# Kernel tuning notes

Measured on AMD Instinct MI355X. Metric: run time of the kernel, lower is better.

## Reference

```python
import jax, jax.numpy as jnp
import numpy as np

NUM_HEADS = 16
HEAD_DIM = 64
Q_DIM = K_DIM = V_DIM = 1024
LQ = LK = 4096
TAU = HEAD_DIM ** (-0.5)


def setup_inputs() -> dict:
    key = jax.random.key(0)
    ks = jax.random.split(key, 11)
    inner = NUM_HEADS * HEAD_DIM
    s = 0.02
    return {
        "q": jax.random.normal(ks[0], (LQ, Q_DIM), dtype=jnp.float32),
        "k": jax.random.normal(ks[1], (LK, K_DIM), dtype=jnp.float32),
        "v": jax.random.normal(ks[2], (LK, V_DIM), dtype=jnp.float32),
        "Wq": jax.random.normal(ks[3], (Q_DIM, inner), dtype=jnp.float32) * s,
        "bq": jax.random.normal(ks[4], (inner,), dtype=jnp.float32) * s,
        "Wk": jax.random.normal(ks[5], (K_DIM, inner), dtype=jnp.float32) * s,
        "bk": jax.random.normal(ks[6], (inner,), dtype=jnp.float32) * s,
        "Wv": jax.random.normal(ks[7], (V_DIM, inner), dtype=jnp.float32) * s,
        "bv": jax.random.normal(ks[8], (inner,), dtype=jnp.float32) * s,
        "Wo": jax.random.normal(ks[9], (inner, Q_DIM), dtype=jnp.float32) * s,
        "bo": jax.random.normal(ks[10], (Q_DIM,), dtype=jnp.float32) * s,
    }


def reference(q, k, v, Wq, bq, Wk, bk, Wv, bv, Wo, bo):
    h, x = NUM_HEADS, HEAD_DIM
    # projections: [L, h*x] -> per-head layout
    qh = (q @ Wq + bq).reshape(-1, h, x)  # [Lq, h, x]
    kh = (k @ Wk + bk).reshape(-1, h, x)  # [Lk, h, x]
    vh = (v @ Wv + bv).reshape(-1, h, x)  # [Lk, h, x]
    # scores: [h, Lq, Lk]
    att = jnp.einsum('qhx,khx->hqk', qh, kh) * TAU
    att = jax.nn.softmax(att, axis=-1)  # dropout=0.0 -> identity
    ctx = jnp.einsum('hqk,khx->qhx', att, vh).reshape(-1, h * x)  # [Lq, h*x]
    out = ctx @ Wo + bo  # [Lq, Q_DIM]
    return out, att
```

## Files before the change

kernel.cpp:

```cpp
#include <hip/hip_runtime.h>
#include <hip/hip_bf16.h>

typedef unsigned short ushort_t;
typedef __attribute__((ext_vector_type(8))) short short8;
typedef __attribute__((ext_vector_type(8))) __bf16 bf16x8;
typedef __attribute__((ext_vector_type(4))) float f32x4;

#define LQS 4096
#define LKS 4096
#define NH 16
#define HD 64
#define DIN 1024
#define KVB 64
static constexpr float TAU_S = 0.125f;
static constexpr float LOG2E = 1.4426950408889634f;

__device__ __forceinline__ float exp2_fast(float x) { return __builtin_amdgcn_exp2f(x); }
__device__ __forceinline__ float log2_fast(float x) { return __builtin_amdgcn_logf(x); }

__device__ __forceinline__ ushort_t f32_to_bf16(float x) {
  union { float f; unsigned u; } v; v.f = x;
  unsigned r = v.u + 0x7FFF + ((v.u >> 16) & 1);
  return (ushort_t)(r >> 16);
}

__device__ __forceinline__ unsigned cvt_pk_bf16(float a, float b) {
  unsigned r;
  asm volatile("v_cvt_pk_bf16_f32 %0, %1, %2" : "=v"(r) : "v"(a), "v"(b));
  return r;
}

__device__ __forceinline__ void gld_lds16(const void* g, void* l) {
  __builtin_amdgcn_global_load_lds((const __attribute__((address_space(1))) void*)g,
                                   (__attribute__((address_space(3))) void*)l, 16, 0, 0);
}

__device__ __forceinline__ f32x4 mfma16(bf16x8 a, bf16x8 b, f32x4 c) {
  return __builtin_amdgcn_mfma_f32_16x16x32_bf16(a, b, c, 0, 0, 0);
}

struct Cvt3 { const float* src[3]; ushort_t* dst[3]; };
__global__ void cvt_kernel(Cvt3 c) {
  const float* __restrict__ src = c.src[blockIdx.y];
  ushort_t* __restrict__ dst = c.dst[blockIdx.y];
  int i = (blockIdx.x * 256 + threadIdx.x) * 8;
  float4 a = *(const float4*)(src + i);
  float4 b = *(const float4*)(src + i + 4);
  union { unsigned w[4]; short8 s; } o;
  o.w[0] = cvt_pk_bf16(a.x, a.y);
  o.w[1] = cvt_pk_bf16(a.z, a.w);
  o.w[2] = cvt_pk_bf16(b.x, b.y);
  o.w[3] = cvt_pk_bf16(b.z, b.w);
  *(short8*)(dst + i) = o.s;
}

struct TW4 { const float* W[4]; ushort_t* Wt[4]; };
__global__ void transpose_w(TW4 w) {
  const float* __restrict__ W = w.W[blockIdx.z];
  ushort_t* __restrict__ Wt = w.Wt[blockIdx.z];
  __shared__ float tile[64][65];
  const int t = threadIdx.x;
  const int k0 = blockIdx.y * 64, n0 = blockIdx.x * 64;
#pragma unroll
  for (int i = 0; i < 16; ++i) {
    int idx = i * 256 + t;
    int r = idx >> 6, c = idx & 63;
    tile[r][c] = W[(size_t)(k0 + r) * DIN + n0 + c];
  }
  __syncthreads();
#pragma unroll
  for (int i = 0; i < 16; ++i) {
    int idx = i * 256 + t;
    int r = idx >> 6, c = idx & 63;
    Wt[(size_t)(n0 + r) * DIN + k0 + c] = f32_to_bf16(tile[c][r]);
  }
}

__global__ void transpose_v(const ushort_t* __restrict__ vh, ushort_t* __restrict__ vt) {
  __shared__ ushort_t tile[64][65];
  const int t = threadIdx.x;
  const int k0 = blockIdx.x * 64, h = blockIdx.y;
#pragma unroll
  for (int i = 0; i < 16; ++i) {
    int idx = i * 256 + t;
    int r = idx >> 6, c = idx & 63;
    tile[r][c] = vh[(size_t)(k0 + r) * DIN + h * HD + c];
  }
  __syncthreads();
#pragma unroll
  for (int i = 0; i < 16; ++i) {
    int idx = i * 256 + t;
    int r = idx >> 6, c = idx & 63;
    vt[((size_t)h * HD + r) * (size_t)LKS + k0 + c] = tile[c][r];
  }
}

struct Batch3 {
  const ushort_t* A[3];
  const ushort_t* Bt[3];
  const float* bias[3];
  void* C[3];
  float scale[3];
};
template <bool OUT_F32>
__launch_bounds__(256, 2)
__global__ void gemm_nt(Batch3 bt3) {
  const int bid = blockIdx.x;
  const int xcd = bid & 7, idx = bid >> 3;
  const int z = idx >> 5, rem = idx & 31;
  const int by = xcd * 4 + (rem >> 3), bx = rem & 7;
  const ushort_t* __restrict__ A = bt3.A[z];
  const ushort_t* __restrict__ Bt = bt3.Bt[z];
  const float* __restrict__ bias = bt3.bias[z];
  void* __restrict__ Cout = bt3.C[z];
  const float scale = bt3.scale[z];
  const int K = DIN, N = DIN;

  __shared__ __align__(16) ushort_t Alds[128 * 64];
  __shared__ __align__(16) ushort_t Blds[128 * 64];
  const int t = threadIdx.x, wave = t >> 6, lane = t & 63;
  const int l15 = lane & 15, lg = lane >> 4;
  const int m0 = by * 128, n0 = bx * 128;
  const int wr = wave >> 1, wc = wave & 1;
  f32x4 acc[4][4];
#pragma unroll
  for (int i = 0; i < 4; ++i)
#pragma unroll
    for (int j = 0; j < 4; ++j) acc[i][j] = (f32x4){0.f, 0.f, 0.f, 0.f};

  for (int tk = 0; tk < K / 64; ++tk) {
#pragma unroll
    for (int c = 0; c < 4; ++c) {
      int chunk = wave * 4 + c;
      int row = chunk * 8 + (lane >> 3);
      int ss = (lane & 7) ^ (row & 7);
      gld_lds16(A + (size_t)(m0 + row) * K + tk * 64 + ss * 8, (char*)Alds + chunk * 1024);
      gld_lds16(Bt + (size_t)(n0 + row) * K + tk * 64 + ss * 8, (char*)Blds + chunk * 1024);
    }
    __syncthreads();
#pragma unroll
    for (int kk = 0; kk < 2; ++kk) {
      bf16x8 a[4], b[4];
#pragma unroll
      for (int i = 0; i < 4; ++i) {
        int ra = wr * 64 + i * 16 + l15;
        a[i] = *(const bf16x8*)((const char*)Alds + ra * 128 + ((((kk * 4 + lg) << 4)) ^ ((ra & 7) << 4)));
        int rb = wc * 64 + i * 16 + l15;
        b[i] = *(const bf16x8*)((const char*)Blds + rb * 128 + ((((kk * 4 + lg) << 4)) ^ ((rb & 7) << 4)));
      }
#pragma unroll
      for (int mi = 0; mi < 4; ++mi)
#pragma unroll
        for (int ni = 0; ni < 4; ++ni)
          acc[mi][ni] = mfma16(a[mi], b[ni], acc[mi][ni]);
    }
    __syncthreads();
  }
#pragma unroll
  for (int ni = 0; ni < 4; ++ni) {
    int coln = n0 + wc * 64 + ni * 16 + l15;
    float bv = bias[coln];
#pragma unroll
    for (int mi = 0; mi < 4; ++mi) {
#pragma unroll
      for (int r = 0; r < 4; ++r) {
        int rowm = m0 + wr * 64 + mi * 16 + lg * 4 + r;
        float v = (acc[mi][ni][r] + bv) * scale;
        if (OUT_F32)
          ((float*)Cout)[(size_t)rowm * N + coln] = v;
        else
          ((ushort_t*)Cout)[(size_t)rowm * N + coln] = f32_to_bf16(v);
      }
    }
  }
}

__launch_bounds__(256, 2)
__global__ void attn_kernel(const ushort_t* __restrict__ qh, const ushort_t* __restrict__ kh,
                            const ushort_t* __restrict__ vt, float* __restrict__ att,
                            ushort_t* __restrict__ ctx) {
  __shared__ __align__(16) ushort_t Klds[2][KVB * 64];
  __shared__ __align__(16) ushort_t Vlds[2][KVB * 64];
  const int t = threadIdx.x, wave = t >> 6, lane = t & 63;
  const int l15 = lane & 15, lg = lane >> 4;
  const int bid = blockIdx.x;
  const int xcd = bid & 7, idx = bid >> 3;
  const int h = xcd * 2 + (idx >> 5);
  const int q0 = (idx & 31) * 128;
  const int w0 = q0 + wave * 32;

  bf16x8 qa[2][2];
#pragma unroll
  for (int g = 0; g < 2; ++g) {
    const ushort_t* qp = qh + (size_t)(w0 + g * 16 + l15) * DIN + h * HD + lg * 8;
    qa[g][0] = *(const bf16x8*)(qp);
    qa[g][1] = *(const bf16x8*)(qp + 32);
  }

  const int srow8 = lane >> 3;
  const int sslot = (lane & 7);

  float rs[2] = {0.f, 0.f};
  for (int tk = 0; tk < LKS / (2 * KVB); ++tk) {
#pragma unroll
    for (int sub = 0; sub < 2; ++sub) {
#pragma unroll
      for (int c = 0; c < 2; ++c) {
        int chunk = wave * 2 + c;
        int row = chunk * 8 + srow8;
        int ss = sslot ^ (row & 7);
        gld_lds16(kh + (size_t)((tk * 2 + sub) * KVB + row) * DIN + h * HD + ss * 8,
                  (char*)Klds[sub] + chunk * 1024);
      }
    }
    __syncthreads();
#pragma unroll
    for (int sub = 0; sub < 2; ++sub) {
#pragma unroll
      for (int ct = 0; ct < 4; ++ct) {
        f32x4 a0 = (f32x4){0.f, 0.f, 0.f, 0.f};
        f32x4 a1 = (f32x4){0.f, 0.f, 0.f, 0.f};
#pragma unroll
        for (int kk = 0; kk < 2; ++kk) {
          int row = ct * 16 + l15;
          bf16x8 kb = *(const bf16x8*)((const char*)Klds[sub] + row * 128 + ((((kk * 4 + lg) << 4)) ^ ((row & 7) << 4)));
          a0 = mfma16(kb, qa[0][kk], a0);
          a1 = mfma16(kb, qa[1][kk], a1);
        }
#pragma unroll
        for (int r = 0; r < 4; ++r) {
          rs[0] += exp2_fast(a0[r]);
          rs[1] += exp2_fast(a1[r]);
        }
      }
    }
    __syncthreads();
  }
  float lrs[2];
#pragma unroll
  for (int g = 0; g < 2; ++g) {
    rs[g] += __shfl_xor(rs[g], 16, 64);
    rs[g] += __shfl_xor(rs[g], 32, 64);
    lrs[g] = log2_fast(rs[g]);
  }

  f32x4 cacc[2][4];
#pragma unroll
  for (int g = 0; g < 2; ++g)
#pragma unroll
    for (int x = 0; x < 4; ++x) cacc[g][x] = (f32x4){0.f, 0.f, 0.f, 0.f};
  float* atth = att + ((size_t)h << 24);

  for (int tk = 0; tk < LKS / (2 * KVB); ++tk) {
#pragma unroll
    for (int sub = 0; sub < 2; ++sub) {
#pragma unroll
      for (int c = 0; c < 2; ++c) {
        int chunk = wave * 2 + c;
        int row = chunk * 8 + srow8;
        int ss = sslot ^ (row & 7);
        gld_lds16(kh + (size_t)((tk * 2 + sub) * KVB + row) * DIN + h * HD + ss * 8,
                  (char*)Klds[sub] + chunk * 1024);
        gld_lds16(vt + ((size_t)h * HD + row) * (size_t)LKS + (tk * 2 + sub) * KVB + ss * 8,
                  (char*)Vlds[sub] + chunk * 1024);
      }
    }
    __syncthreads();
#pragma unroll
    for (int sub = 0; sub < 2; ++sub) {
      float p[2][4][4];
#pragma unroll
      for (int ct = 0; ct < 4; ++ct) {
        f32x4 a0 = (f32x4){0.f, 0.f, 0.f, 0.f};
        f32x4 a1 = (f32x4){0.f, 0.f, 0.f, 0.f};
#pragma unroll
        for (int kk = 0; kk < 2; ++kk) {
          int row = ct * 16 + l15;
          bf16x8 kb = *(const bf16x8*)((const char*)Klds[sub] + row * 128 + ((((kk * 4 + lg) << 4)) ^ ((row & 7) << 4)));
          a0 = mfma16(kb, qa[0][kk], a0);
          a1 = mfma16(kb, qa[1][kk], a1);
        }
#pragma unroll
        for (int r = 0; r < 4; ++r) {
          p[0][ct][r] = exp2_fast(a0[r] - lrs[0]);
          p[1][ct][r] = exp2_fast(a1[r] - lrs[1]);
        }
      }
#pragma unroll
      for (int g = 0; g < 2; ++g) {
#pragma unroll
        for (int ct = 0; ct < 4; ++ct) {
          f32x4 v = (f32x4){p[g][ct][0], p[g][ct][1], p[g][ct][2], p[g][ct][3]};
          *(f32x4*)(atth + (((size_t)(w0 + g * 16 + l15)) << 12) + (tk * 2 + sub) * KVB + ct * 16 + lg * 4) = v;
        }
      }
      bf16x8 pa[2][2];
#pragma unroll
      for (int g = 0; g < 2; ++g)
#pragma unroll
        for (int kk = 0; kk < 2; ++kk) {
          union { unsigned w[4]; bf16x8 v; } P;
          P.w[0] = cvt_pk_bf16(p[g][2 * kk][0], p[g][2 * kk][1]);
          P.w[1] = cvt_pk_bf16(p[g][2 * kk][2], p[g][2 * kk][3]);
          P.w[2] = cvt_pk_bf16(p[g][2 * kk + 1][0], p[g][2 * kk + 1][1]);
          P.w[3] = cvt_pk_bf16(p[g][2 * kk + 1][2], p[g][2 * kk + 1][3]);
          pa[g][kk] = P.v;
        }
#pragma unroll
      for (int x = 0; x < 4; ++x) {
        int row = x * 16 + l15;
        const char* vrow = (const char*)Vlds[sub] + row * 128;
        int par = row & 7;
        int sb = (lg & 1) << 3;
#pragma unroll
        for (int kk = 0; kk < 2; ++kk) {
          int sA = (4 * kk + (lg >> 1)) ^ par;
          int sB = (4 * kk + 2 + (lg >> 1)) ^ par;
          union { unsigned long long q[2]; bf16x8 v; } U;
          U.q[0] = *(const unsigned long long*)(vrow + (sA << 4) + sb);
          U.q[1] = *(const unsigned long long*)(vrow + (sB << 4) + sb);
          cacc[0][x] = mfma16(pa[0][kk], U.v, cacc[0][x]);
          cacc[1][x] = mfma16(pa[1][kk], U.v, cacc[1][x]);
        }
      }
    }
    __syncthreads();
  }
#pragma unroll
  for (int g = 0; g < 2; ++g)
#pragma unroll
    for (int x = 0; x < 4; ++x) {
#pragma unroll
      for (int r = 0; r < 4; ++r) {
        int rowq = w0 + g * 16 + lg * 4 + r;
        int col = h * HD + x * 16 + l15;
        ctx[(size_t)rowq * DIN + col] = f32_to_bf16(cacc[g][x][r]);
      }
    }
}

extern "C" void kernel_launch(void* const* d_in, const int* in_sizes, int n_in,
                              void* d_out, int out_size, void* d_ws, size_t ws_size,
                              hipStream_t stream) {
  const float* q = (const float*)d_in[0];
  const float* k = (const float*)d_in[1];
  const float* v = (const float*)d_in[2];
  const float* Wq = (const float*)d_in[3];
  const float* bq = (const float*)d_in[4];
  const float* Wk = (const float*)d_in[5];
  const float* bk = (const float*)d_in[6];
  const float* Wv = (const float*)d_in[7];
  const float* bv = (const float*)d_in[8];
  const float* Wo = (const float*)d_in[9];
  const float* bo = (const float*)d_in[10];

  float* out = (float*)d_out;
  float* att = out + (size_t)LQS * DIN;

  char* ws = (char*)d_ws;
  ushort_t* qhb = (ushort_t*)(ws + (size_t)0);
  ushort_t* khb = (ushort_t*)(ws + ((size_t)8 << 20));
  ushort_t* vhb = (ushort_t*)(ws + ((size_t)16 << 20));
  ushort_t* vtb = (ushort_t*)(ws + ((size_t)24 << 20));
  ushort_t* ctx = (ushort_t*)(ws + ((size_t)32 << 20));
  ushort_t* qb = (ushort_t*)(ws + ((size_t)40 << 20));
  ushort_t* kb = (ushort_t*)(ws + ((size_t)48 << 20));
  ushort_t* vb = (ushort_t*)(ws + ((size_t)56 << 20));
  ushort_t* Wqt = (ushort_t*)(ws + ((size_t)64 << 20));
  ushort_t* Wkt = (ushort_t*)(ws + ((size_t)66 << 20));
  ushort_t* Wvt = (ushort_t*)(ws + ((size_t)68 << 20));
  ushort_t* Wot = (ushort_t*)(ws + ((size_t)70 << 20));

  Cvt3 c3;
  c3.src[0] = q; c3.src[1] = k; c3.src[2] = v;
  c3.dst[0] = qb; c3.dst[1] = kb; c3.dst[2] = vb;
  cvt_kernel<<<dim3(LQS * DIN / 8 / 256, 3), 256, 0, stream>>>(c3);

  TW4 w4;
  w4.W[0] = Wq; w4.W[1] = Wk; w4.W[2] = Wv; w4.W[3] = Wo;
  w4.Wt[0] = Wqt; w4.Wt[1] = Wkt; w4.Wt[2] = Wvt; w4.Wt[3] = Wot;
  transpose_w<<<dim3(16, 16, 4), 256, 0, stream>>>(w4);

  Batch3 pb;
  pb.A[0] = qb; pb.A[1] = kb; pb.A[2] = vb;
  pb.Bt[0] = Wqt; pb.Bt[1] = Wkt; pb.Bt[2] = Wvt;
  pb.bias[0] = bq; pb.bias[1] = bk; pb.bias[2] = bv;
  pb.C[0] = qhb; pb.C[1] = khb; pb.C[2] = vhb;
  pb.scale[0] = TAU_S * LOG2E; pb.scale[1] = 1.0f; pb.scale[2] = 1.0f;
  gemm_nt<false><<<768, 256, 0, stream>>>(pb);

  transpose_v<<<dim3(64, 16), 256, 0, stream>>>(vhb, vtb);

  attn_kernel<<<512, 256, 0, stream>>>(qhb, khb, vtb, att, ctx);

  Batch3 ob;
  ob.A[0] = ctx; ob.A[1] = ctx; ob.A[2] = ctx;
  ob.Bt[0] = Wot; ob.Bt[1] = Wot; ob.Bt[2] = Wot;
  ob.bias[0] = bo; ob.bias[1] = bo; ob.bias[2] = bo;
  ob.C[0] = out; ob.C[1] = out; ob.C[2] = out;
  ob.scale[0] = 1.0f; ob.scale[1] = 1.0f; ob.scale[2] = 1.0f;
  gemm_nt<true><<<256, 256, 0, stream>>>(ob);
}
```

Before: 391.6 us.

## Double-buffer K/V tiles and give each wave 64 query rows in attention

The attention kernel now stages the next K (and V) tile into the alternate LDS buffer while computing on the current one, replacing the previous load-then-sync pattern. Each wave handles 64 query rows instead of 32, so each K/V tile loaded into LDS is reused across twice as many rows, and the grid shrinks from 512 to 256 blocks. Launch bounds drop to one block per CU to allow the extra registers. This reduces K/V reloads and exposes less memory latency, at the cost of lower occupancy and a grid of only 256 blocks, which may leave some CUs idle on a large GPU.

```diff
diff --git a/kernel.cpp b/kernel.cpp
--- a/kernel.cpp
+++ b/kernel.cpp
@@ -175,7 +175,7 @@
   }
 }
 
-__launch_bounds__(256, 2)
+__launch_bounds__(256, 1)
 __global__ void attn_kernel(const ushort_t* __restrict__ qh, const ushort_t* __restrict__ kh,
                             const ushort_t* __restrict__ vt, float* __restrict__ att,
                             ushort_t* __restrict__ ctx) {
@@ -185,13 +185,13 @@
   const int l15 = lane & 15, lg = lane >> 4;
   const int bid = blockIdx.x;
   const int xcd = bid & 7, idx = bid >> 3;
-  const int h = xcd * 2 + (idx >> 5);
-  const int q0 = (idx & 31) * 128;
-  const int w0 = q0 + wave * 32;
-
-  bf16x8 qa[2][2];
-#pragma unroll
-  for (int g = 0; g < 2; ++g) {
+  const int h = xcd * 2 + (idx >> 4);
+  const int q0 = (idx & 15) * 256;
+  const int w0 = q0 + wave * 64;
+
+  bf16x8 qa[4][2];
+#pragma unroll
+  for (int g = 0; g < 4; ++g) {
     const ushort_t* qp = qh + (size_t)(w0 + g * 16 + l15) * DIN + h * HD + lg * 8;
     qa[g][0] = *(const bf16x8*)(qp);
     qa[g][1] = *(const bf16x8*)(qp + 32);
@@ -199,135 +199,142 @@
 
   const int srow8 = lane >> 3;
   const int sslot = (lane & 7);
-
-  float rs[2] = {0.f, 0.f};
-  for (int tk = 0; tk < LKS / (2 * KVB); ++tk) {
-#pragma unroll
-    for (int sub = 0; sub < 2; ++sub) {
-#pragma unroll
-      for (int c = 0; c < 2; ++c) {
-        int chunk = wave * 2 + c;
-        int row = chunk * 8 + srow8;
-        int ss = sslot ^ (row & 7);
-        gld_lds16(kh + (size_t)((tk * 2 + sub) * KVB + row) * DIN + h * HD + ss * 8,
-                  (char*)Klds[sub] + chunk * 1024);
-      }
+  const int NT = LKS / KVB;
+
+#define STAGE_K(tile, buf)                                                          \
+  {                                                                                 \
+    _Pragma("unroll") for (int c = 0; c < 2; ++c) {                                 \
+      int chunk = wave * 2 + c;                                                     \
+      int row = chunk * 8 + srow8;                                                  \
+      int ss = sslot ^ (row & 7);                                                   \
+      gld_lds16(kh + (size_t)((tile) * KVB + row) * DIN + h * HD + ss * 8,          \
+                (char*)Klds[buf] + chunk * 1024);                                   \
+    }                                                                               \
+  }
+#define STAGE_V(tile, buf)                                                          \
+  {                                                                                 \
+    _Pragma("unroll") for (int c = 0; c < 2; ++c) {                                 \
+      int chunk = wave * 2 + c;                                                     \
+      int row = chunk * 8 + srow8;                                                  \
+      int ss = sslot ^ (row & 7);                                                   \
+      gld_lds16(vt + ((size_t)h * HD + row) * (size_t)LKS + (tile) * KVB + ss * 8,  \
+                (char*)Vlds[buf] + chunk * 1024);                                   \
+    }                                                                               \
+  }
+
+  float rs[4] = {0.f, 0.f, 0.f, 0.f};
+  STAGE_K(0, 0);
+  __syncthreads();
+  int cur = 0;
+  for (int tk = 0; tk < NT; ++tk) {
+    if (tk + 1 < NT) STAGE_K(tk + 1, cur ^ 1);
+#pragma unroll
+    for (int ct = 0; ct < 4; ++ct) {
+      int row = ct * 16 + l15;
+      bf16x8 kb0 = *(const bf16x8*)((const char*)Klds[cur] + row * 128 + (((lg << 4)) ^ ((row & 7) << 4)));
+      bf16x8 kb1 = *(const bf16x8*)((const char*)Klds[cur] + row * 128 + ((((4 + lg) << 4)) ^ ((row & 7) << 4)));
+      f32x4 a[4];
+#pragma unroll
+      for (int g = 0; g < 4; ++g) {
+        a[g] = mfma16(kb0, qa[g][0], (f32x4){0.f, 0.f, 0.f, 0.f});
+        a[g] = mfma16(kb1, qa[g][1], a[g]);
+      }
+#pragma unroll
+      for (int g = 0; g < 4; ++g)
+#pragma unroll
+        for (int r = 0; r < 4; ++r) rs[g] += exp2_fast(a[g][r]);
     }
     __syncthreads();
-#pragma unroll
-    for (int sub = 0; sub < 2; ++sub) {
-#pragma unroll
-      for (int ct = 0; ct < 4; ++ct) {
-        f32x4 a0 = (f32x4){0.f, 0.f, 0.f, 0.f};
-        f32x4 a1 = (f32x4){0.f, 0.f, 0.f, 0.f};
-#pragma unroll
-        for (int kk = 0; kk < 2; ++kk) {
-          int row = ct * 16 + l15;
-          bf16x8 kb = *(const bf16x8*)((const char*)Klds[sub] + row * 128 + ((((kk * 4 + lg) << 4)) ^ ((row & 7) << 4)));
-          a0 = mfma16(kb, qa[0][kk], a0);
-          a1 = mfma16(kb, qa[1][kk], a1);
-        }
-#pragma unroll
-        for (int r = 0; r < 4; ++r) {
-          rs[0] += exp2_fast(a0[r]);
-          rs[1] += exp2_fast(a1[r]);
-        }
-      }
-    }
-    __syncthreads();
-  }
-  float lrs[2];
-#pragma unroll
-  for (int g = 0; g < 2; ++g) {
+    cur ^= 1;
+  }
+  float lrs[4];
+#pragma unroll
+  for (int g = 0; g < 4; ++g) {
     rs[g] += __shfl_xor(rs[g], 16, 64);
     rs[g] += __shfl_xor(rs[g], 32, 64);
     lrs[g] = log2_fast(rs[g]);
   }
 
-  f32x4 cacc[2][4];
-#pragma unroll
-  for (int g = 0; g < 2; ++g)
+  f32x4 cacc[4][4];
+#pragma unroll
+  for (int g = 0; g < 4; ++g)
 #pragma unroll
     for (int x = 0; x < 4; ++x) cacc[g][x] = (f32x4){0.f, 0.f, 0.f, 0.f};
   float* atth = att + ((size_t)h << 24);
 
-  for (int tk = 0; tk < LKS / (2 * KVB); ++tk) {
-#pragma unroll
-    for (int sub = 0; sub < 2; ++sub) {
-#pragma unroll
-      for (int c = 0; c < 2; ++c) {
-        int chunk = wave * 2 + c;
-        int row = chunk * 8 + srow8;
-        int ss = sslot ^ (row & 7);
-        gld_lds16(kh + (size_t)((tk * 2 + sub) * KVB + row) * DIN + h * HD + ss * 8,
-                  (char*)Klds[sub] + chunk * 1024);
-        gld_lds16(vt + ((size_t)h * HD + row) * (size_t)LKS + (tk * 2 + sub) * KVB + ss * 8,
-                  (char*)Vlds[sub] + chunk * 1024);
+  STAGE_K(0, 0);
+  STAGE_V(0, 0);
+  __syncthreads();
+  cur = 0;
+  for (int tk = 0; tk < NT; ++tk) {
+    if (tk + 1 < NT) {
+      STAGE_K(tk + 1, cur ^ 1);
+      STAGE_V(tk + 1, cur ^ 1);
+    }
+    bf16x8 pa[4][2];
+    float pprev[4][4];
+#pragma unroll
+    for (int ct = 0; ct < 4; ++ct) {
+      int row = ct * 16 + l15;
+      bf16x8 kb0 = *(const bf16x8*)((const char*)Klds[cur] + row * 128 + (((lg << 4)) ^ ((row & 7) << 4)));
+      bf16x8 kb1 = *(const bf16x8*)((const char*)Klds[cur] + row * 128 + ((((4 + lg) << 4)) ^ ((row & 7) << 4)));
+      f32x4 a[4];
+#pragma unroll
+      for (int g = 0; g < 4; ++g) {
+        a[g] = mfma16(kb0, qa[g][0], (f32x4){0.f, 0.f, 0.f, 0.f});
+        a[g] = mfma16(kb1, qa[g][1], a[g]);
+      }
+      float pcur[4][4];
+#pragma unroll
+      for (int g = 0; g < 4; ++g)
+#pragma unroll
+        for (int r = 0; r < 4; ++r) pcur[g][r] = exp2_fast(a[g][r] - lrs[g]);
+#pragma unroll
+      for (int g = 0; g < 4; ++g) {
+        f32x4 v = (f32x4){pcur[g][0], pcur[g][1], pcur[g][2], pcur[g][3]};
+        *(f32x4*)(atth + (((size_t)(w0 + g * 16 + l15)) << 12) + tk * KVB + ct * 16 + lg * 4) = v;
+      }
+      if (ct & 1) {
+#pragma unroll
+        for (int g = 0; g < 4; ++g) {
+          union { unsigned w[4]; bf16x8 v; } P;
+          P.w[0] = cvt_pk_bf16(pprev[g][0], pprev[g][1]);
+          P.w[1] = cvt_pk_bf16(pprev[g][2], pprev[g][3]);
+          P.w[2] = cvt_pk_bf16(pcur[g][0], pcur[g][1]);
+          P.w[3] = cvt_pk_bf16(pcur[g][2], pcur[g][3]);
+          pa[g][ct >> 1] = P.v;
+        }
+      } else {
+#pragma unroll
+        for (int g = 0; g < 4; ++g)
+#pragma unroll
+          for (int r = 0; r < 4; ++r) pprev[g][r] = pcur[g][r];
+      }
+    }
+#pragma unroll
+    for (int x = 0; x < 4; ++x) {
+      int row = x * 16 + l15;
+      const char* vrow = (const char*)Vlds[cur] + row * 128;
+      int par = row & 7;
+      int sb = (lg & 1) << 3;
+#pragma unroll
+      for (int kk = 0; kk < 2; ++kk) {
+        int sA = (4 * kk + (lg >> 1)) ^ par;
+        int sB = (4 * kk + 2 + (lg >> 1)) ^ par;
+        union { unsigned long long q[2]; bf16x8 v; } U;
+        U.q[0] = *(const unsigned long long*)(vrow + (sA << 4) + sb);
+        U.q[1] = *(const unsigned long long*)(vrow + (sB << 4) + sb);
+#pragma unroll
+        for (int g = 0; g < 4; ++g) cacc[g][x] = mfma16(pa[g][kk], U.v, cacc[g][x]);
       }
     }
     __syncthreads();
-#pragma unroll
-    for (int sub = 0; sub < 2; ++sub) {
-      float p[2][4][4];
-#pragma unroll
-      for (int ct = 0; ct < 4; ++ct) {
-        f32x4 a0 = (f32x4){0.f, 0.f, 0.f, 0.f};
-        f32x4 a1 = (f32x4){0.f, 0.f, 0.f, 0.f};
-#pragma unroll
-        for (int kk = 0; kk < 2; ++kk) {
-          int row = ct * 16 + l15;
-          bf16x8 kb = *(const bf16x8*)((const char*)Klds[sub] + row * 128 + ((((kk * 4 + lg) << 4)) ^ ((row & 7) << 4)));
-          a0 = mfma16(kb, qa[0][kk], a0);
-          a1 = mfma16(kb, qa[1][kk], a1);
-        }
-#pragma unroll
-        for (int r = 0; r < 4; ++r) {
-          p[0][ct][r] = exp2_fast(a0[r] - lrs[0]);
-          p[1][ct][r] = exp2_fast(a1[r] - lrs[1]);
-        }
-      }
-#pragma unroll
-      for (int g = 0; g < 2; ++g) {
-#pragma unroll
-        for (int ct = 0; ct < 4; ++ct) {
-          f32x4 v = (f32x4){p[g][ct][0], p[g][ct][1], p[g][ct][2], p[g][ct][3]};
-          *(f32x4*)(atth + (((size_t)(w0 + g * 16 + l15)) << 12) + (tk * 2 + sub) * KVB + ct * 16 + lg * 4) = v;
-        }
-      }
-      bf16x8 pa[2][2];
-#pragma unroll
-      for (int g = 0; g < 2; ++g)
-#pragma unroll
-        for (int kk = 0; kk < 2; ++kk) {
-          union { unsigned w[4]; bf16x8 v; } P;
-          P.w[0] = cvt_pk_bf16(p[g][2 * kk][0], p[g][2 * kk][1]);
-          P.w[1] = cvt_pk_bf16(p[g][2 * kk][2], p[g][2 * kk][3]);
-          P.w[2] = cvt_pk_bf16(p[g][2 * kk + 1][0], p[g][2 * kk + 1][1]);
-          P.w[3] = cvt_pk_bf16(p[g][2 * kk + 1][2], p[g][2 * kk + 1][3]);
-          pa[g][kk] = P.v;
-        }
-#pragma unroll
-      for (int x = 0; x < 4; ++x) {
-        int row = x * 16 + l15;
-        const char* vrow = (const char*)Vlds[sub] + row * 128;
-        int par = row & 7;
-        int sb = (lg & 1) << 3;
-#pragma unroll
-        for (int kk = 0; kk < 2; ++kk) {
-          int sA = (4 * kk + (lg >> 1)) ^ par;
-          int sB = (4 * kk + 2 + (lg >> 1)) ^ par;
-          union { unsigned long long q[2]; bf16x8 v; } U;
-          U.q[0] = *(const unsigned long long*)(vrow + (sA << 4) + sb);
-          U.q[1] = *(const unsigned long long*)(vrow + (sB << 4) + sb);
-          cacc[0][x] = mfma16(pa[0][kk], U.v, cacc[0][x]);
-          cacc[1][x] = mfma16(pa[1][kk], U.v, cacc[1][x]);
-        }
-      }
-    }
-    __syncthreads();
-  }
-#pragma unroll
-  for (int g = 0; g < 2; ++g)
+    cur ^= 1;
+  }
+#undef STAGE_K
+#undef STAGE_V
+#pragma unroll
+  for (int g = 0; g < 4; ++g)
 #pragma unroll
     for (int x = 0; x < 4; ++x) {
 #pragma unroll
@@ -391,7 +398,7 @@
 
   transpose_v<<<dim3(64, 16), 256, 0, stream>>>(vhb, vtb);
 
-  attn_kernel<<<512, 256, 0, stream>>>(qhb, khb, vtb, att, ctx);
+  attn_kernel<<<256, 256, 0, stream>>>(qhb, khb, vtb, att, ctx);
 
   Batch3 ob;
   ob.A[0] = ctx; ob.A[1] = ctx; ob.A[2] = ctx;
```

Result: slower. 554.8 us (+41.7%).

## Split softmax row-sum pass into separate kernel with larger Q tiles and split-K

Applied to the files above, without the earlier changes.

Moves the first pass of attention, which computes softmax denominators without max subtraction, out of attn_kernel into a new rowsum_kernel. Each wave now handles 64 query rows, so every loaded K tile feeds more MFMAs. Each block covers half of the key range, with the two partial sums written to a workspace buffer. The new kernel also double-buffers K loads into shared memory so the next tile loads during compute. attn_kernel reads the two partial sums and takes their log, at the cost of one more launch and a small global buffer.

```diff
diff --git a/kernel.cpp b/kernel.cpp
--- a/kernel.cpp
+++ b/kernel.cpp
@@ -176,9 +176,84 @@
 }
 
 __launch_bounds__(256, 2)
+__global__ void rowsum_kernel(const ushort_t* __restrict__ qh, const ushort_t* __restrict__ kh,
+                              float* __restrict__ rsbuf) {
+  __shared__ __align__(16) ushort_t Klds[2][KVB * 64];
+  const int t = threadIdx.x, wave = t >> 6, lane = t & 63;
+  const int l15 = lane & 15, lg = lane >> 4;
+  const int bid = blockIdx.x;
+  const int xcd = bid & 7, idx = bid >> 3;
+  const int h = xcd * 2 + (idx >> 5);
+  const int rem = idx & 31;
+  const int q0 = (rem >> 1) * 256;
+  const int half = rem & 1;
+  const int w0 = q0 + wave * 64;
+
+  bf16x8 qa[4][2];
+#pragma unroll
+  for (int g = 0; g < 4; ++g) {
+    const ushort_t* qp = qh + (size_t)(w0 + g * 16 + l15) * DIN + h * HD + lg * 8;
+    qa[g][0] = *(const bf16x8*)(qp);
+    qa[g][1] = *(const bf16x8*)(qp + 32);
+  }
+
+  const int srow8 = lane >> 3;
+  const int sslot = (lane & 7);
+  const int tk0 = half * 32;
+
+#define STAGE_K1(tile, buf)                                                         \
+  {                                                                                 \
+    _Pragma("unroll") for (int c = 0; c < 2; ++c) {                                 \
+      int chunk = wave * 2 + c;                                                     \
+      int row = chunk * 8 + srow8;                                                  \
+      int ss = sslot ^ (row & 7);                                                   \
+      gld_lds16(kh + (size_t)((tile) * KVB + row) * DIN + h * HD + ss * 8,          \
+                (char*)Klds[buf] + chunk * 1024);                                   \
+    }                                                                               \
+  }
+
+  float rs[4] = {0.f, 0.f, 0.f, 0.f};
+  STAGE_K1(tk0, 0);
+  __syncthreads();
+  int cur = 0;
+  for (int tk = 0; tk < 32; ++tk) {
+    if (tk + 1 < 32) STAGE_K1(tk0 + tk + 1, cur ^ 1);
+#pragma unroll
+    for (int ct = 0; ct < 4; ++ct) {
+      int row = ct * 16 + l15;
+      bf16x8 kb0 = *(const bf16x8*)((const char*)Klds[cur] + row * 128 + (((lg << 4)) ^ ((row & 7) << 4)));
+      bf16x8 kb1 = *(const bf16x8*)((const char*)Klds[cur] + row * 128 + ((((4 + lg) << 4)) ^ ((row & 7) << 4)));
+      f32x4 a[4];
+#pragma unroll
+      for (int g = 0; g < 4; ++g) {
+        a[g] = mfma16(kb0, qa[g][0], (f32x4){0.f, 0.f, 0.f, 0.f});
+        a[g] = mfma16(kb1, qa[g][1], a[g]);
+      }
+#pragma unroll
+      for (int g = 0; g < 4; ++g)
+#pragma unroll
+        for (int r = 0; r < 4; ++r) rs[g] += exp2_fast(a[g][r]);
+    }
+    __syncthreads();
+    cur ^= 1;
+  }
+#undef STAGE_K1
+#pragma unroll
+  for (int g = 0; g < 4; ++g) {
+    rs[g] += __shfl_xor(rs[g], 16, 64);
+    rs[g] += __shfl_xor(rs[g], 32, 64);
+  }
+  if (lg == 0) {
+#pragma unroll
+    for (int g = 0; g < 4; ++g)
+      rsbuf[(((size_t)half * NH + h) << 12) + w0 + g * 16 + l15] = rs[g];
+  }
+}
+
+__launch_bounds__(256, 2)
 __global__ void attn_kernel(const ushort_t* __restrict__ qh, const ushort_t* __restrict__ kh,
-                            const ushort_t* __restrict__ vt, float* __restrict__ att,
-                            ushort_t* __restrict__ ctx) {
+                            const ushort_t* __restrict__ vt, const float* __restrict__ rsbuf,
+                            float* __restrict__ att, ushort_t* __restrict__ ctx) {
   __shared__ __align__(16) ushort_t Klds[2][KVB * 64];
   __shared__ __align__(16) ushort_t Vlds[2][KVB * 64];
   const int t = threadIdx.x, wave = t >> 6, lane = t & 63;
@@ -197,52 +272,16 @@
     qa[g][1] = *(const bf16x8*)(qp + 32);
   }
 
+  float lrs[2];
+#pragma unroll
+  for (int g = 0; g < 2; ++g) {
+    size_t row = (size_t)w0 + g * 16 + l15;
+    float ps = rsbuf[((size_t)h << 12) + row] + rsbuf[(((size_t)NH + h) << 12) + row];
+    lrs[g] = log2_fast(ps);
+  }
+
   const int srow8 = lane >> 3;
   const int sslot = (lane & 7);
-
-  float rs[2] = {0.f, 0.f};
-  for (int tk = 0; tk < LKS / (2 * KVB); ++tk) {
-#pragma unroll
-    for (int sub = 0; sub < 2; ++sub) {
-#pragma unroll
-      for (int c = 0; c < 2; ++c) {
-        int chunk = wave * 2 + c;
-        int row = chunk * 8 + srow8;
-        int ss = sslot ^ (row & 7);
-        gld_lds16(kh + (size_t)((tk * 2 + sub) * KVB + row) * DIN + h * HD + ss * 8,
-                  (char*)Klds[sub] + chunk * 1024);
-      }
-    }
-    __syncthreads();
-#pragma unroll
-    for (int sub = 0; sub < 2; ++sub) {
-#pragma unroll
-      for (int ct = 0; ct < 4; ++ct) {
-        f32x4 a0 = (f32x4){0.f, 0.f, 0.f, 0.f};
-        f32x4 a1 = (f32x4){0.f, 0.f, 0.f, 0.f};
-#pragma unroll
-        for (int kk = 0; kk < 2; ++kk) {
-          int row = ct * 16 + l15;
-          bf16x8 kb = *(const bf16x8*)((const char*)Klds[sub] + row * 128 + ((((kk * 4 + lg) << 4)) ^ ((row & 7) << 4)));
-          a0 = mfma16(kb, qa[0][kk], a0);
-          a1 = mfma16(kb, qa[1][kk], a1);
-        }
-#pragma unroll
-        for (int r = 0; r < 4; ++r) {
-          rs[0] += exp2_fast(a0[r]);
-          rs[1] += exp2_fast(a1[r]);
-        }
-      }
-    }
-    __syncthreads();
-  }
-  float lrs[2];
-#pragma unroll
-  for (int g = 0; g < 2; ++g) {
-    rs[g] += __shfl_xor(rs[g], 16, 64);
-    rs[g] += __shfl_xor(rs[g], 32, 64);
-    lrs[g] = log2_fast(rs[g]);
-  }
 
   f32x4 cacc[2][4];
 #pragma unroll
@@ -370,6 +409,7 @@
   ushort_t* Wkt = (ushort_t*)(ws + ((size_t)66 << 20));
   ushort_t* Wvt = (ushort_t*)(ws + ((size_t)68 << 20));
   ushort_t* Wot = (ushort_t*)(ws + ((size_t)70 << 20));
+  float* rsbuf = (float*)(ws + ((size_t)72 << 20));
 
   Cvt3 c3;
   c3.src[0] = q; c3.src[1] = k; c3.src[2] = v;
@@ -389,9 +429,11 @@
   pb.scale[0] = TAU_S * LOG2E; pb.scale[1] = 1.0f; pb.scale[2] = 1.0f;
   gemm_nt<false><<<768, 256, 0, stream>>>(pb);
 
+  rowsum_kernel<<<512, 256, 0, stream>>>(qhb, khb, rsbuf);
+
   transpose_v<<<dim3(64, 16), 256, 0, stream>>>(vhb, vtb);
 
-  attn_kernel<<<512, 256, 0, stream>>>(qhb, khb, vtb, att, ctx);
+  attn_kernel<<<512, 256, 0, stream>>>(qhb, khb, vtb, rsbuf, att, ctx);
 
   Batch3 ob;
   ob.A[0] = ctx; ob.A[1] = ctx; ob.A[2] = ctx;
```

Result: no change. 385.9 us (-1.5%).
